# Kernel tuning notes

Measured on AMD Instinct MI355X. Metric: run time of the kernel, lower is better.

The kernel has to match this reference:

```python
import jax, jax.numpy as jnp
import numpy as np

NUM_ITERATIONS = 3
EPS = 1e-08


def _squash(s):
    # s: [B, D]
    s_norm = jnp.linalg.norm(s, axis=-1, keepdims=True)
    scale = s_norm ** 2 / (1.0 + s_norm ** 2) / (s_norm + EPS)
    return scale * s


def setup_inputs() -> dict:
    key = jax.random.key(0)
    capsule_outputs = jax.random.normal(key, (16384, 64, 64), dtype=jnp.float32)
    return {"capsule_outputs": capsule_outputs}


def reference(capsule_outputs):
    # capsule_outputs: [B, N, D]
    B, N, _ = capsule_outputs.shape
    b = jnp.zeros((B, N, 1), dtype=capsule_outputs.dtype)
    v = None
    for it in range(NUM_ITERATIONS):
        c = jax.nn.softmax(b, axis=1)               # [B, N, 1]
        s = jnp.sum(c * capsule_outputs, axis=1)    # [B, D]
        v = _squash(s)                              # [B, D]
        if it < NUM_ITERATIONS - 1:
            # agreement: dot(capsule_outputs[b,n,:], v[b,:]) -> [B, N, 1]
            agreement = jnp.sum(capsule_outputs * v[:, None, :], axis=2, keepdims=True)
            b = b + agreement
    return v
```

## Files before the change

### kernel.cpp

```cpp
#include <hip/hip_runtime.h>
#include <hip/hip_bf16.h>


__global__ __launch_bounds__(256)
void routing_kernel(const float* __restrict__ X, float* __restrict__ out, int B) {
    const int w = (blockIdx.x << 2) + (threadIdx.x >> 6);
    if (w >= B) return;
    const int l = threadIdx.x & 63;
    const int g = l & 15;

    const float* Xb = X + (size_t)w * 4096;

    float4 data[16];
    #pragma unroll
    for (int i = 0; i < 16; ++i)
        data[i] = *reinterpret_cast<const float4*>(Xb + i * 256 + 4 * l);

    float blog[16];
    #pragma unroll
    for (int i = 0; i < 16; ++i) blog[i] = 0.0f;

    float c[16];
    float4 v4 = make_float4(0.f, 0.f, 0.f, 0.f);

    for (int it = 0; it < 3; ++it) {
        float4 s4;
        if (it == 0) {
            s4 = make_float4(0.f, 0.f, 0.f, 0.f);
            #pragma unroll
            for (int i = 0; i < 16; ++i) {
                s4.x += data[i].x; s4.y += data[i].y;
                s4.z += data[i].z; s4.w += data[i].w;
            }
            s4.x *= 0.015625f; s4.y *= 0.015625f; s4.z *= 0.015625f; s4.w *= 0.015625f;
        } else {
            float m = blog[0];
            #pragma unroll
            for (int i = 1; i < 16; ++i) m = fmaxf(m, blog[i]);
            m = fmaxf(m, __shfl_xor(m, 16));
            m = fmaxf(m, __shfl_xor(m, 32));
            float sum = 0.0f;
            #pragma unroll
            for (int i = 0; i < 16; ++i) { c[i] = __expf(blog[i] - m); sum += c[i]; }
            sum += __shfl_xor(sum, 16);
            sum += __shfl_xor(sum, 32);
            const float r = 1.0f / sum;
            #pragma unroll
            for (int i = 0; i < 16; ++i) c[i] *= r;

            s4 = make_float4(0.f, 0.f, 0.f, 0.f);
            #pragma unroll
            for (int i = 0; i < 16; ++i) {
                s4.x = fmaf(c[i], data[i].x, s4.x);
                s4.y = fmaf(c[i], data[i].y, s4.y);
                s4.z = fmaf(c[i], data[i].z, s4.z);
                s4.w = fmaf(c[i], data[i].w, s4.w);
            }
        }
        #pragma unroll
        for (int off = 16; off <= 32; off <<= 1) {
            s4.x += __shfl_xor(s4.x, off);
            s4.y += __shfl_xor(s4.y, off);
            s4.z += __shfl_xor(s4.z, off);
            s4.w += __shfl_xor(s4.w, off);
        }

        float n2 = s4.x * s4.x + s4.y * s4.y + s4.z * s4.z + s4.w * s4.w;
        #pragma unroll
        for (int off = 1; off <= 8; off <<= 1) n2 += __shfl_xor(n2, off);
        const float norm = sqrtf(n2);
        const float scale = n2 / (1.0f + n2) / (norm + 1e-8f);
        v4.x = scale * s4.x; v4.y = scale * s4.y;
        v4.z = scale * s4.z; v4.w = scale * s4.w;

        if (it < 2) {
            #pragma unroll
            for (int i = 0; i < 16; ++i) {
                float a = data[i].x * v4.x + data[i].y * v4.y
                        + data[i].z * v4.z + data[i].w * v4.w;
                #pragma unroll
                for (int off = 1; off <= 8; off <<= 1) a += __shfl_xor(a, off);
                blog[i] += a;
            }
        }
    }

    if (l < 16)
        *reinterpret_cast<float4*>(out + (size_t)w * 64 + 4 * g) = v4;
}

extern "C" void kernel_launch(void* const* d_in, const int* in_sizes, int n_in,
                              void* d_out, int out_size, void* d_ws, size_t ws_size,
                              hipStream_t stream) {
    const float* X = (const float*)d_in[0];
    float* out = (float*)d_out;
    const int B = in_sizes[0] / 4096;
    const int blocks = (B + 3) / 4;
    routing_kernel<<<blocks, 256, 0, stream>>>(X, out, B);
}
```

Measured before the change: 48.26 us.

## Make waves persistent over several batch items with double-buffered register prefetch

Each wavefront now handles eight batch elements instead of one. It uses two register buffers so the next element's 16 KB load is issued before the current element's routing math runs. The goal is to hide global-memory latency inside each wave rather than relying only on occupancy. In exchange it needs twice the data registers (launch bounds set to 2 blocks per SM), launches far fewer blocks, and the tail handling logic becomes more complex.

```diff
diff --git a/kernel.cpp b/kernel.cpp
--- a/kernel.cpp
+++ b/kernel.cpp
@@ -2,20 +2,18 @@
 #include <hip/hip_bf16.h>
 
 
-__global__ __launch_bounds__(256)
-void routing_kernel(const float* __restrict__ X, float* __restrict__ out, int B) {
-    const int w = (blockIdx.x << 2) + (threadIdx.x >> 6);
-    if (w >= B) return;
-    const int l = threadIdx.x & 63;
-    const int g = l & 15;
+#define ELEMS 8
 
-    const float* Xb = X + (size_t)w * 4096;
-
-    float4 data[16];
+__device__ __forceinline__ void issue_load(float4 (&buf)[16],
+                                           const float* __restrict__ Xb, int l) {
     #pragma unroll
     for (int i = 0; i < 16; ++i)
-        data[i] = *reinterpret_cast<const float4*>(Xb + i * 256 + 4 * l);
+        buf[i] = *reinterpret_cast<const float4*>(Xb + i * 256 + 4 * l);
+}
 
+__device__ __forceinline__ void process(const float4 (&data)[16],
+                                        float* __restrict__ outp, int l) {
+    const int g = l & 15;
     float blog[16];
     #pragma unroll
     for (int i = 0; i < 16; ++i) blog[i] = 0.0f;
@@ -23,6 +21,7 @@
     float c[16];
     float4 v4 = make_float4(0.f, 0.f, 0.f, 0.f);
 
+    #pragma unroll
     for (int it = 0; it < 3; ++it) {
         float4 s4;
         if (it == 0) {
@@ -32,7 +31,8 @@
                 s4.x += data[i].x; s4.y += data[i].y;
                 s4.z += data[i].z; s4.w += data[i].w;
             }
-            s4.x *= 0.015625f; s4.y *= 0.015625f; s4.z *= 0.015625f; s4.w *= 0.015625f;
+            s4.x *= 0.015625f; s4.y *= 0.015625f;
+            s4.z *= 0.015625f; s4.w *= 0.015625f;
         } else {
             float m = blog[0];
             #pragma unroll
@@ -64,7 +64,6 @@
             s4.z += __shfl_xor(s4.z, off);
             s4.w += __shfl_xor(s4.w, off);
         }
-
         float n2 = s4.x * s4.x + s4.y * s4.y + s4.z * s4.z + s4.w * s4.w;
         #pragma unroll
         for (int off = 1; off <= 8; off <<= 1) n2 += __shfl_xor(n2, off);
@@ -86,7 +85,32 @@
     }
 
     if (l < 16)
-        *reinterpret_cast<float4*>(out + (size_t)w * 64 + 4 * g) = v4;
+        *reinterpret_cast<float4*>(outp + 4 * g) = v4;
+}
+
+__global__ __launch_bounds__(256, 2)
+void routing_kernel(const float* __restrict__ X, float* __restrict__ out, int B) {
+    const int wid = (blockIdx.x << 2) + (threadIdx.x >> 6);
+    const int l = threadIdx.x & 63;
+    const int base = wid * ELEMS;
+    if (base >= B) return;
+
+    float4 bufA[16], bufB[16];
+
+    issue_load(bufA, X + (size_t)base * 4096, l);
+
+    #pragma unroll 1
+    for (int e = 0; e < ELEMS; e += 2) {
+        const int elem = base + e;
+        const bool has1 = (elem + 1 < B);
+        const bool has2 = has1 && (e + 2 < ELEMS) && (elem + 2 < B);
+
+        if (has1) issue_load(bufB, X + (size_t)(elem + 1) * 4096, l);
+        process(bufA, out + (size_t)elem * 64, l);
+        if (has2) issue_load(bufA, X + (size_t)(elem + 2) * 4096, l);
+        if (has1) process(bufB, out + (size_t)(elem + 1) * 64, l);
+        if (elem + 2 >= B) break;
+    }
 }
 
 extern "C" void kernel_launch(void* const* d_in, const int* in_sizes, int n_in,
@@ -95,6 +119,7 @@
     const float* X = (const float*)d_in[0];
     float* out = (float*)d_out;
     const int B = in_sizes[0] / 4096;
-    const int blocks = (B + 3) / 4;
+    const int waves = (B + ELEMS - 1) / ELEMS;
+    const int blocks = (waves + 3) / 4;
     routing_kernel<<<blocks, 256, 0, stream>>>(X, out, B);
 }
```

After: 58.55 us. 21.3% more time.

## Make waves persistent over 8 batches with async global-to-LDS prefetch

Applied to the files above, without the earlier changes.

Each wave now handles 8 consecutive batch elements instead of one. It stages each 16 KB tile into LDS with global_load_lds DMA and issues the next element's DMA right after copying the current tile into registers, so the load overlaps the routing compute. The softmax normalization is also folded so the reciprocal is applied after the weighted sum. In exchange it uses 64 KB of LDS per block, which limits occupancy, and launches 8x fewer waves, which may reduce the memory-level parallelism this bandwidth-bound kernel depends on.

```diff
diff --git a/kernel.cpp b/kernel.cpp
--- a/kernel.cpp
+++ b/kernel.cpp
@@ -2,91 +2,126 @@
 #include <hip/hip_bf16.h>
 
 
-__global__ __launch_bounds__(256)
+#define ELEMS 8
+#define WPB   4
+
+__device__ __forceinline__ void dma_tile(const float* __restrict__ gbase,
+                                         float* lbuf, int l) {
+    #pragma unroll
+    for (int i = 0; i < 16; ++i) {
+        __builtin_amdgcn_global_load_lds(
+            (const __attribute__((address_space(1))) void*)(gbase + i * 256 + 4 * l),
+            (__attribute__((address_space(3))) void*)(lbuf + i * 256),
+            16, 0, 0);
+    }
+}
+
+__global__ __launch_bounds__(256, 2)
 void routing_kernel(const float* __restrict__ X, float* __restrict__ out, int B) {
-    const int w = (blockIdx.x << 2) + (threadIdx.x >> 6);
-    if (w >= B) return;
-    const int l = threadIdx.x & 63;
-    const int g = l & 15;
+    __shared__ float lds[WPB][4096];
+    const int wv = threadIdx.x >> 6;
+    const int l  = threadIdx.x & 63;
+    const int g  = l & 15;
+    float* buf = lds[wv];
 
-    const float* Xb = X + (size_t)w * 4096;
+    const long base = ((long)blockIdx.x * WPB + wv) * ELEMS;
+    if (base >= B) return;
 
-    float4 data[16];
-    #pragma unroll
-    for (int i = 0; i < 16; ++i)
-        data[i] = *reinterpret_cast<const float4*>(Xb + i * 256 + 4 * l);
+    dma_tile(X + base * 4096, buf, l);
 
-    float blog[16];
-    #pragma unroll
-    for (int i = 0; i < 16; ++i) blog[i] = 0.0f;
+    #pragma unroll 1
+    for (int e = 0; e < ELEMS; ++e) {
+        const long elem = base + e;
+        if (elem >= B) break;
 
-    float c[16];
-    float4 v4 = make_float4(0.f, 0.f, 0.f, 0.f);
+        asm volatile("s_waitcnt vmcnt(0)" ::: "memory");
 
-    for (int it = 0; it < 3; ++it) {
-        float4 s4;
-        if (it == 0) {
-            s4 = make_float4(0.f, 0.f, 0.f, 0.f);
+        float4 data[16];
+        #pragma unroll
+        for (int i = 0; i < 16; ++i)
+            data[i] = *reinterpret_cast<const float4*>(buf + i * 256 + 4 * l);
+
+        asm volatile("s_waitcnt lgkmcnt(0)" ::: "memory");
+        if (e + 1 < ELEMS && elem + 1 < B)
+            dma_tile(X + (elem + 1) * 4096, buf, l);
+
+        float blog[16];
+        #pragma unroll
+        for (int i = 0; i < 16; ++i) blog[i] = 0.0f;
+        float4 v4 = make_float4(0.f, 0.f, 0.f, 0.f);
+
+        #pragma unroll
+        for (int it = 0; it < 3; ++it) {
+            float4 s4;
+            if (it == 0) {
+                s4 = make_float4(0.f, 0.f, 0.f, 0.f);
+                #pragma unroll
+                for (int i = 0; i < 16; ++i) {
+                    s4.x += data[i].x; s4.y += data[i].y;
+                    s4.z += data[i].z; s4.w += data[i].w;
+                }
+                s4.x *= 0.015625f; s4.y *= 0.015625f;
+                s4.z *= 0.015625f; s4.w *= 0.015625f;
+                #pragma unroll
+                for (int off = 16; off <= 32; off <<= 1) {
+                    s4.x += __shfl_xor(s4.x, off);
+                    s4.y += __shfl_xor(s4.y, off);
+                    s4.z += __shfl_xor(s4.z, off);
+                    s4.w += __shfl_xor(s4.w, off);
+                }
+            } else {
+                float m = blog[0];
+                #pragma unroll
+                for (int i = 1; i < 16; ++i) m = fmaxf(m, blog[i]);
+                m = fmaxf(m, __shfl_xor(m, 16));
+                m = fmaxf(m, __shfl_xor(m, 32));
+                float sum = 0.0f;
+                s4 = make_float4(0.f, 0.f, 0.f, 0.f);
+                #pragma unroll
+                for (int i = 0; i < 16; ++i) {
+                    const float ei = __expf(blog[i] - m);
+                    sum += ei;
+                    s4.x = fmaf(ei, data[i].x, s4.x);
+                    s4.y = fmaf(ei, data[i].y, s4.y);
+                    s4.z = fmaf(ei, data[i].z, s4.z);
+                    s4.w = fmaf(ei, data[i].w, s4.w);
+                }
+                sum += __shfl_xor(sum, 16);
+                sum += __shfl_xor(sum, 32);
+                #pragma unroll
+                for (int off = 16; off <= 32; off <<= 1) {
+                    s4.x += __shfl_xor(s4.x, off);
+                    s4.y += __shfl_xor(s4.y, off);
+                    s4.z += __shfl_xor(s4.z, off);
+                    s4.w += __shfl_xor(s4.w, off);
+                }
+                const float r = 1.0f / sum;
+                s4.x *= r; s4.y *= r; s4.z *= r; s4.w *= r;
+            }
+
+            float n2 = s4.x * s4.x + s4.y * s4.y + s4.z * s4.z + s4.w * s4.w;
             #pragma unroll
-            for (int i = 0; i < 16; ++i) {
-                s4.x += data[i].x; s4.y += data[i].y;
-                s4.z += data[i].z; s4.w += data[i].w;
-            }
-            s4.x *= 0.015625f; s4.y *= 0.015625f; s4.z *= 0.015625f; s4.w *= 0.015625f;
-        } else {
-            float m = blog[0];
-            #pragma unroll
-            for (int i = 1; i < 16; ++i) m = fmaxf(m, blog[i]);
-            m = fmaxf(m, __shfl_xor(m, 16));
-            m = fmaxf(m, __shfl_xor(m, 32));
-            float sum = 0.0f;
-            #pragma unroll
-            for (int i = 0; i < 16; ++i) { c[i] = __expf(blog[i] - m); sum += c[i]; }
-            sum += __shfl_xor(sum, 16);
-            sum += __shfl_xor(sum, 32);
-            const float r = 1.0f / sum;
-            #pragma unroll
-            for (int i = 0; i < 16; ++i) c[i] *= r;
+            for (int off = 1; off <= 8; off <<= 1) n2 += __shfl_xor(n2, off);
+            const float norm = sqrtf(n2);
+            const float scale = n2 / (1.0f + n2) / (norm + 1e-8f);
+            v4.x = scale * s4.x; v4.y = scale * s4.y;
+            v4.z = scale * s4.z; v4.w = scale * s4.w;
 
-            s4 = make_float4(0.f, 0.f, 0.f, 0.f);
-            #pragma unroll
-            for (int i = 0; i < 16; ++i) {
-                s4.x = fmaf(c[i], data[i].x, s4.x);
-                s4.y = fmaf(c[i], data[i].y, s4.y);
-                s4.z = fmaf(c[i], data[i].z, s4.z);
-                s4.w = fmaf(c[i], data[i].w, s4.w);
+            if (it < 2) {
+                #pragma unroll
+                for (int i = 0; i < 16; ++i) {
+                    float a = data[i].x * v4.x + data[i].y * v4.y
+                            + data[i].z * v4.z + data[i].w * v4.w;
+                    #pragma unroll
+                    for (int off = 1; off <= 8; off <<= 1) a += __shfl_xor(a, off);
+                    blog[i] += a;
+                }
             }
         }
-        #pragma unroll
-        for (int off = 16; off <= 32; off <<= 1) {
-            s4.x += __shfl_xor(s4.x, off);
-            s4.y += __shfl_xor(s4.y, off);
-            s4.z += __shfl_xor(s4.z, off);
-            s4.w += __shfl_xor(s4.w, off);
-        }
 
-        float n2 = s4.x * s4.x + s4.y * s4.y + s4.z * s4.z + s4.w * s4.w;
-        #pragma unroll
-        for (int off = 1; off <= 8; off <<= 1) n2 += __shfl_xor(n2, off);
-        const float norm = sqrtf(n2);
-        const float scale = n2 / (1.0f + n2) / (norm + 1e-8f);
-        v4.x = scale * s4.x; v4.y = scale * s4.y;
-        v4.z = scale * s4.z; v4.w = scale * s4.w;
-
-        if (it < 2) {
-            #pragma unroll
-            for (int i = 0; i < 16; ++i) {
-                float a = data[i].x * v4.x + data[i].y * v4.y
-                        + data[i].z * v4.z + data[i].w * v4.w;
-                #pragma unroll
-                for (int off = 1; off <= 8; off <<= 1) a += __shfl_xor(a, off);
-                blog[i] += a;
-            }
-        }
+        if (l < 16)
+            *reinterpret_cast<float4*>(out + elem * 64 + 4 * g) = v4;
     }
-
-    if (l < 16)
-        *reinterpret_cast<float4*>(out + (size_t)w * 64 + 4 * g) = v4;
 }
 
 extern "C" void kernel_launch(void* const* d_in, const int* in_sizes, int n_in,
@@ -95,6 +130,7 @@
     const float* X = (const float*)d_in[0];
     float* out = (float*)d_out;
     const int B = in_sizes[0] / 4096;
-    const int blocks = (B + 3) / 4;
+    const int waves = (B + ELEMS - 1) / ELEMS;
+    const int blocks = (waves + WPB - 1) / WPB;
     routing_kernel<<<blocks, 256, 0, stream>>>(X, out, B);
 }
```

Result: slower. 61.72 us (+27.9%).

## Process four batch elements per wave with nontemporal loads and fused softmax-sum

Applied to the files above, without the earlier changes.

Each wavefront now loops serially over four batch elements instead of handling one, so the grid is a quarter the size. Loads and stores use nontemporal builtins to bypass cache retention for the streamed input. The softmax normalization is folded into the weighted sum, scaling once at the end instead of per coefficient. The risk is lower memory-level parallelism: there are fewer waves in flight, and the unroll-1 loop serializes the loads of consecutive elements within a wave.

```diff
diff --git a/kernel.cpp b/kernel.cpp
--- a/kernel.cpp
+++ b/kernel.cpp
@@ -2,91 +2,92 @@
 #include <hip/hip_bf16.h>
 
 
+#define ELEMS 4
+
+typedef float __attribute__((ext_vector_type(4))) f32x4;
+
+__device__ __forceinline__ f32x4 shfl_xor4(f32x4 v, int m) {
+    f32x4 r;
+    r[0] = __shfl_xor(v[0], m);
+    r[1] = __shfl_xor(v[1], m);
+    r[2] = __shfl_xor(v[2], m);
+    r[3] = __shfl_xor(v[3], m);
+    return r;
+}
+
 __global__ __launch_bounds__(256)
 void routing_kernel(const float* __restrict__ X, float* __restrict__ out, int B) {
-    const int w = (blockIdx.x << 2) + (threadIdx.x >> 6);
-    if (w >= B) return;
+    const int wid = (blockIdx.x << 2) + (threadIdx.x >> 6);
     const int l = threadIdx.x & 63;
     const int g = l & 15;
 
-    const float* Xb = X + (size_t)w * 4096;
+    #pragma unroll 1
+    for (int e = 0; e < ELEMS; ++e) {
+        const long elem = (long)wid * ELEMS + e;
+        if (elem >= B) break;
 
-    float4 data[16];
-    #pragma unroll
-    for (int i = 0; i < 16; ++i)
-        data[i] = *reinterpret_cast<const float4*>(Xb + i * 256 + 4 * l);
+        const f32x4* Xb = reinterpret_cast<const f32x4*>(X + elem * 4096) + l;
+        f32x4 data[16];
+        #pragma unroll
+        for (int i = 0; i < 16; ++i)
+            data[i] = __builtin_nontemporal_load(Xb + i * 64);
 
-    float blog[16];
-    #pragma unroll
-    for (int i = 0; i < 16; ++i) blog[i] = 0.0f;
+        float blog[16];
+        #pragma unroll
+        for (int i = 0; i < 16; ++i) blog[i] = 0.0f;
+        f32x4 v4 = (f32x4)0.0f;
 
-    float c[16];
-    float4 v4 = make_float4(0.f, 0.f, 0.f, 0.f);
+        #pragma unroll
+        for (int it = 0; it < 3; ++it) {
+            f32x4 s4 = (f32x4)0.0f;
+            if (it == 0) {
+                #pragma unroll
+                for (int i = 0; i < 16; ++i) s4 += data[i];
+                s4 *= 0.015625f;
+            } else {
+                float m = blog[0];
+                #pragma unroll
+                for (int i = 1; i < 16; ++i) m = fmaxf(m, blog[i]);
+                m = fmaxf(m, __shfl_xor(m, 16));
+                m = fmaxf(m, __shfl_xor(m, 32));
+                float sum = 0.0f;
+                #pragma unroll
+                for (int i = 0; i < 16; ++i) {
+                    const float ei = __expf(blog[i] - m);
+                    sum += ei;
+                    s4 += data[i] * ei;
+                }
+                sum += __shfl_xor(sum, 16);
+                sum += __shfl_xor(sum, 32);
+                const float r = 1.0f / sum;
+                s4 *= r;
+            }
+            s4 += shfl_xor4(s4, 16);
+            s4 += shfl_xor4(s4, 32);
 
-    for (int it = 0; it < 3; ++it) {
-        float4 s4;
-        if (it == 0) {
-            s4 = make_float4(0.f, 0.f, 0.f, 0.f);
+            float n2 = s4[0] * s4[0] + s4[1] * s4[1] + s4[2] * s4[2] + s4[3] * s4[3];
             #pragma unroll
-            for (int i = 0; i < 16; ++i) {
-                s4.x += data[i].x; s4.y += data[i].y;
-                s4.z += data[i].z; s4.w += data[i].w;
-            }
-            s4.x *= 0.015625f; s4.y *= 0.015625f; s4.z *= 0.015625f; s4.w *= 0.015625f;
-        } else {
-            float m = blog[0];
-            #pragma unroll
-            for (int i = 1; i < 16; ++i) m = fmaxf(m, blog[i]);
-            m = fmaxf(m, __shfl_xor(m, 16));
-            m = fmaxf(m, __shfl_xor(m, 32));
-            float sum = 0.0f;
-            #pragma unroll
-            for (int i = 0; i < 16; ++i) { c[i] = __expf(blog[i] - m); sum += c[i]; }
-            sum += __shfl_xor(sum, 16);
-            sum += __shfl_xor(sum, 32);
-            const float r = 1.0f / sum;
-            #pragma unroll
-            for (int i = 0; i < 16; ++i) c[i] *= r;
+            for (int off = 1; off <= 8; off <<= 1) n2 += __shfl_xor(n2, off);
+            const float norm = sqrtf(n2);
+            const float scale = n2 / (1.0f + n2) / (norm + 1e-8f);
+            v4 = s4 * scale;
 
-            s4 = make_float4(0.f, 0.f, 0.f, 0.f);
-            #pragma unroll
-            for (int i = 0; i < 16; ++i) {
-                s4.x = fmaf(c[i], data[i].x, s4.x);
-                s4.y = fmaf(c[i], data[i].y, s4.y);
-                s4.z = fmaf(c[i], data[i].z, s4.z);
-                s4.w = fmaf(c[i], data[i].w, s4.w);
+            if (it < 2) {
+                #pragma unroll
+                for (int i = 0; i < 16; ++i) {
+                    f32x4 t = data[i] * v4;
+                    float a = t[0] + t[1] + t[2] + t[3];
+                    #pragma unroll
+                    for (int off = 1; off <= 8; off <<= 1) a += __shfl_xor(a, off);
+                    blog[i] += a;
+                }
             }
         }
-        #pragma unroll
-        for (int off = 16; off <= 32; off <<= 1) {
-            s4.x += __shfl_xor(s4.x, off);
-            s4.y += __shfl_xor(s4.y, off);
-            s4.z += __shfl_xor(s4.z, off);
-            s4.w += __shfl_xor(s4.w, off);
-        }
 
-        float n2 = s4.x * s4.x + s4.y * s4.y + s4.z * s4.z + s4.w * s4.w;
-        #pragma unroll
-        for (int off = 1; off <= 8; off <<= 1) n2 += __shfl_xor(n2, off);
-        const float norm = sqrtf(n2);
-        const float scale = n2 / (1.0f + n2) / (norm + 1e-8f);
-        v4.x = scale * s4.x; v4.y = scale * s4.y;
-        v4.z = scale * s4.z; v4.w = scale * s4.w;
-
-        if (it < 2) {
-            #pragma unroll
-            for (int i = 0; i < 16; ++i) {
-                float a = data[i].x * v4.x + data[i].y * v4.y
-                        + data[i].z * v4.z + data[i].w * v4.w;
-                #pragma unroll
-                for (int off = 1; off <= 8; off <<= 1) a += __shfl_xor(a, off);
-                blog[i] += a;
-            }
-        }
+        if (l < 16)
+            __builtin_nontemporal_store(
+                v4, reinterpret_cast<f32x4*>(out + elem * 64) + g);
     }
-
-    if (l < 16)
-        *reinterpret_cast<float4*>(out + (size_t)w * 64 + 4 * g) = v4;
 }
 
 extern "C" void kernel_launch(void* const* d_in, const int* in_sizes, int n_in,
@@ -95,6 +96,7 @@
     const float* X = (const float*)d_in[0];
     float* out = (float*)d_out;
     const int B = in_sizes[0] / 4096;
-    const int blocks = (B + 3) / 4;
+    const int waves = (B + ELEMS - 1) / ELEMS;
+    const int blocks = (waves + 3) / 4;
     routing_kernel<<<blocks, 256, 0, stream>>>(X, out, B);
 }
```

After: 61.05 us. 1.27x slower.
